# Kernel tuning notes

Measured on AMD Instinct MI355X. Metric: run time of the kernel, lower is better.

Reference implementation:

```python
import jax, jax.numpy as jnp
import numpy as np

POOL_SCALES = (1, 2, 3, 6)
MAX_SCALE = 6


def _seq_ppm(x, w, b):
    """SequencePPM: per-frame PPM with per-frame/per-scale 1x1 conv + ReLU.
    x: [T,B,C,H,W]; w: [T,S,Co,C]; b: [T,S,Co]. Returns [T,B,S*Co,MAX,MAX]."""
    T, B, C, H, W = x.shape
    outs = []
    for si, s in enumerate(POOL_SCALES):
        # AdaptiveAvgPool2d(s): H,W divisible by s -> equal block means
        pooled = x.reshape(T, B, C, s, H // s, s, W // s).mean(axis=(4, 6))  # [T,B,C,s,s]
        conv = jnp.einsum('tbcij,toc->tboij', pooled, w[:, si]) + b[:, si][:, None, :, None, None]
        conv = jax.nn.relu(conv)
        # bilinear upsample to (MAX_SCALE, MAX_SCALE), align_corners=False
        up = jax.image.resize(conv, (T, B, conv.shape[2], MAX_SCALE, MAX_SCALE), method='bilinear')
        outs.append(up)
    return jnp.concatenate(outs, axis=2)  # [T,B,sum(Co),MAX,MAX]


def setup_inputs() -> dict:
    key = jax.random.key(0)
    ks = jax.random.split(key, 8)
    T, B, Ck, Cv, H, W = 4, 2, 256, 512, 96, 96
    S = len(POOL_SCALES)
    return {
        'memory_keys': jax.random.normal(ks[0], (T, B, Ck, H, W), jnp.float32),
        'memory_values': jax.random.normal(ks[1], (T, B, Cv, H, W), jnp.float32),
        'query_key': jax.random.normal(ks[2], (B, Ck, H, W), jnp.float32),
        'query_value': jax.random.normal(ks[3], (B, Cv, H, W), jnp.float32),
        'key_w': jax.random.normal(ks[4], (T, S, Ck // S, Ck), jnp.float32) * (Ck ** -0.5),
        'key_b': jnp.zeros((T, S, Ck // S), jnp.float32),
        'val_w': jax.random.normal(ks[5], (T, S, Cv // S, Cv), jnp.float32) * (Cv ** -0.5),
        'val_b': jnp.zeros((T, S, Cv // S), jnp.float32),
    }


def reference(memory_keys, memory_values, query_key, query_value, key_w, key_b, val_w, val_b):
    T, B, Ck, H, W = memory_keys.shape
    Cv = memory_values.shape[2]
    mk = _seq_ppm(memory_keys, key_w, key_b)      # [T,B,Ck,6,6]
    mv = _seq_ppm(memory_values, val_w, val_b)    # [T,B,Cv,6,6]
    h = w = MAX_SCALE
    M = T * h * w
    # keys: [B, M, Ck] with M ordered (T, h, w)
    mk = jnp.transpose(mk, (1, 0, 3, 4, 2)).reshape(B, M, Ck)
    mv = jnp.transpose(mv, (1, 2, 0, 3, 4)).reshape(B, Cv, M)
    qk = query_key.reshape(B, Ck, H * W)
    att = jnp.einsum('bmc,bcn->bmn', mk, qk) * (Ck ** -0.5)  # matmul_norm=True
    att = jax.nn.softmax(att, axis=1)  # softmax over memory dim M
    mem = jnp.einsum('bvm,bmn->bvn', mv, att).reshape(B, Cv, H, W)
    return jnp.concatenate([query_value, mem], axis=1)  # [B, 2*Cv, H, W]
```

## Files before the change

### kernel.cpp

```cpp
#include <hip/hip_runtime.h>
#include <hip/hip_bf16.h>

#define T_ 4
#define B_ 2
#define CK 256
#define CV 512
#define HH 96
#define WW 96
#define NPIX (HH*WW)
#define M_ 144
#define MP 160

typedef __attribute__((ext_vector_type(8))) short short8;
typedef __attribute__((ext_vector_type(4))) float floatx4;

__device__ __forceinline__ unsigned short f2bf(float f) {
    unsigned int u = __float_as_uint(f);
    u += 0x7FFFu + ((u >> 16) & 1u);
    return (unsigned short)(u >> 16);
}

__global__ __launch_bounds__(256) void pool_kernel(
        const float* __restrict__ keys, const float* __restrict__ vals,
        float* __restrict__ pooledK, float* __restrict__ pooledV) {
    int pid = blockIdx.x;
    const float* src; float* dst;
    if (pid < T_*B_*CK) { src = keys + (size_t)pid * NPIX; dst = pooledK + (size_t)pid * 50; }
    else { int p = pid - T_*B_*CK; src = vals + (size_t)p * NPIX; dst = pooledV + (size_t)p * 50; }

    __shared__ float cm[36];
    int tid = threadIdx.x;
    int wv = tid >> 6, lane = tid & 63;
    int r = lane >> 2, c4 = lane & 3;
    #pragma unroll
    for (int g = 0; g < 9; ++g) {
        int cell = g*4 + wv;
        int cr = cell / 6, cc = cell % 6;
        const float4 v = *reinterpret_cast<const float4*>(src + (cr*16 + r)*WW + cc*16 + c4*4);
        float s = v.x + v.y + v.z + v.w;
        #pragma unroll
        for (int m = 1; m < 64; m <<= 1) s += __shfl_xor(s, m);
        if (lane == 0) cm[cell] = s * (1.0f/256.0f);
    }
    __syncthreads();
    if (tid < 50) {
        float v;
        if (tid == 0) {
            float a = 0.f;
            #pragma unroll
            for (int i = 0; i < 36; ++i) a += cm[i];
            v = a * (1.0f/36.0f);
        } else if (tid < 5) {
            int k = tid - 1; int i = k >> 1, j = k & 1;
            float a = 0.f;
            for (int di = 0; di < 3; ++di)
                for (int dj = 0; dj < 3; ++dj) a += cm[(i*3+di)*6 + (j*3+dj)];
            v = a * (1.0f/9.0f);
        } else if (tid < 14) {
            int k = tid - 5; int i = k / 3, j = k % 3;
            float a = 0.f;
            for (int di = 0; di < 2; ++di)
                for (int dj = 0; dj < 2; ++dj) a += cm[(i*2+di)*6 + (j*2+dj)];
            v = a * 0.25f;
        } else {
            v = cm[tid - 14];
        }
        dst[tid] = v;
    }
}

__global__ __launch_bounds__(256) void conv_kernel(
        const float* __restrict__ pooledK, const float* __restrict__ pooledV,
        const float* __restrict__ key_w, const float* __restrict__ key_b,
        const float* __restrict__ val_w, const float* __restrict__ val_b,
        float* __restrict__ convK, float* __restrict__ convV) {
    int gid = blockIdx.x * 4 + (threadIdx.x >> 6);
    int lane = threadIdx.x & 63;
    const int EK = T_*B_*50*64;
    float acc = 0.f;
    if (gid < EK) {
        int co = gid & 63;
        int pos = (gid >> 6) % 50;
        int tb = gid / (64*50);
        int b = tb & 1, t = tb >> 1;
        int si = (pos == 0) ? 0 : (pos < 5 ? 1 : (pos < 14 ? 2 : 3));
        const float* wrow = key_w + (size_t)((t*4 + si)*64 + co) * CK;
        const float* prow = pooledK + (size_t)((t*B_ + b)*CK) * 50 + pos;
        #pragma unroll
        for (int k = 0; k < 4; ++k) {
            int c = lane + 64*k;
            acc += wrow[c] * prow[(size_t)c * 50];
        }
        #pragma unroll
        for (int m = 1; m < 64; m <<= 1) acc += __shfl_xor(acc, m);
        if (lane == 0) convK[gid] = fmaxf(acc + key_b[(t*4 + si)*64 + co], 0.f);
    } else {
        int g2 = gid - EK;
        int co = g2 & 127;
        int pos = (g2 >> 7) % 50;
        int tb = g2 / (128*50);
        int b = tb & 1, t = tb >> 1;
        int si = (pos == 0) ? 0 : (pos < 5 ? 1 : (pos < 14 ? 2 : 3));
        const float* wrow = val_w + (size_t)((t*4 + si)*128 + co) * CV;
        const float* prow = pooledV + (size_t)((t*B_ + b)*CV) * 50 + pos;
        #pragma unroll
        for (int k = 0; k < 8; ++k) {
            int c = lane + 64*k;
            acc += wrow[c] * prow[(size_t)c * 50];
        }
        #pragma unroll
        for (int m = 1; m < 64; m <<= 1) acc += __shfl_xor(acc, m);
        if (lane == 0) convV[g2] = fmaxf(acc + val_b[(t*4 + si)*128 + co], 0.f);
    }
}

__device__ const int   UP_P0[4][6] = {{0,0,0,0,0,0},{0,0,0,0,1,1},{0,0,0,1,1,2},{0,1,2,3,4,5}};
__device__ const int   UP_P1[4][6] = {{0,0,0,0,0,0},{0,0,1,1,1,1},{0,1,1,2,2,2},{0,1,2,3,4,5}};
__device__ const float UP_W0[4][6] = {{1,1,1,1,1,1},
                                      {1,1,0.66666669f,0.33333334f,1,1},
                                      {1,0.75f,0.25f,0.75f,0.25f,1},
                                      {1,1,1,1,1,1}};
__device__ const float UP_W1[4][6] = {{0,0,0,0,0,0},
                                      {0,0,0.33333334f,0.66666669f,0,0},
                                      {0,0.25f,0.75f,0.25f,0.75f,0},
                                      {0,0,0,0,0,0}};
__device__ const int   UP_OFF[4] = {0,1,5,14};
__device__ const int   UP_S[4]   = {1,2,3,6};

__global__ __launch_bounds__(256) void pack_kernel(
        const float* __restrict__ convK, const float* __restrict__ convV,
        unsigned short* __restrict__ mk_b, unsigned short* __restrict__ mv_b) {
    int F = blockIdx.x * 256 + threadIdx.x;
    const int NMK = B_ * M_ * CK;
    if (F < NMK) {
        int c = F & 255;
        int m = (F >> 8) % M_;
        int b = F / (M_ * 256);
        int t = m / 36, rem = m % 36, y = rem / 6, x = rem % 6;
        int si = c >> 6, co = c & 63;
        int s = UP_S[si], off = UP_OFF[si];
        const float* base = convK + (size_t)((t*B_ + b)*50) * 64 + co;
        int py0 = UP_P0[si][y], py1 = UP_P1[si][y];
        int px0 = UP_P0[si][x], px1 = UP_P1[si][x];
        float wy0 = UP_W0[si][y], wy1 = UP_W1[si][y];
        float wx0 = UP_W0[si][x], wx1 = UP_W1[si][x];
        float v = wy0 * (wx0 * base[(off + py0*s + px0)*64] + wx1 * base[(off + py0*s + px1)*64])
                + wy1 * (wx0 * base[(off + py1*s + px0)*64] + wx1 * base[(off + py1*s + px1)*64]);
        mk_b[F] = f2bf(v);
    } else {
        int G = F - NMK;
        int mp = G % MP;
        int cv = (G / MP) % CV;
        int b = G / (MP * CV);
        if (mp >= M_) { mv_b[G] = 0; return; }
        int m = mp;
        int t = m / 36, rem = m % 36, y = rem / 6, x = rem % 6;
        int si = cv >> 7, co = cv & 127;
        int s = UP_S[si], off = UP_OFF[si];
        const float* base = convV + (size_t)((t*B_ + b)*50) * 128 + co;
        int py0 = UP_P0[si][y], py1 = UP_P1[si][y];
        int px0 = UP_P0[si][x], px1 = UP_P1[si][x];
        float wy0 = UP_W0[si][y], wy1 = UP_W1[si][y];
        float wx0 = UP_W0[si][x], wx1 = UP_W1[si][x];
        float v = wy0 * (wx0 * base[(off + py0*s + px0)*128] + wx1 * base[(off + py0*s + px1)*128])
                + wy1 * (wx0 * base[(off + py1*s + px0)*128] + wx1 * base[(off + py1*s + px1)*128]);
        mv_b[G] = f2bf(v);
    }
}

__global__ __launch_bounds__(256) void attn_kernel(
        const float* __restrict__ qk, const float* __restrict__ qv,
        const unsigned short* __restrict__ mk_b, const unsigned short* __restrict__ mv_b,
        float* __restrict__ out) {
    __shared__ __align__(16) unsigned short qk_s[64 * 264];
    __shared__ __align__(16) unsigned short p_s[64 * 168];

    int blk = blockIdx.x;
    int b = blk / 144;
    int n0 = (blk % 144) * 64;
    int tid = threadIdx.x;

    {
        int nn = tid & 63, cq = tid >> 6;
        const float* qb = qk + (size_t)b * CK * NPIX + n0 + nn;
        for (int k = 0; k < 32; ++k) {
            int c0 = 2 * (cq + 4*k);
            float v0 = qb[(size_t)c0 * NPIX];
            float v1 = qb[(size_t)(c0 + 1) * NPIX];
            unsigned int pk = (unsigned int)f2bf(v0) | ((unsigned int)f2bf(v1) << 16);
            *reinterpret_cast<unsigned int*>(&qk_s[nn*264 + c0]) = pk;
        }
    }
    __syncthreads();

    int w = tid >> 6, l = tid & 63;
    int nl = l & 15, q = l >> 4;

    short8 bq[8];
    #pragma unroll
    for (int kt = 0; kt < 8; ++kt)
        bq[kt] = *reinterpret_cast<const short8*>(&qk_s[(w*16 + nl)*264 + kt*32 + q*8]);

    floatx4 sc[9];
    const unsigned short* mkb = mk_b + (size_t)b * M_ * CK + (size_t)nl * CK + q*8;
    #pragma unroll
    for (int mt = 0; mt < 9; ++mt) {
        floatx4 acc = {0.f, 0.f, 0.f, 0.f};
        const unsigned short* ar = mkb + (size_t)mt * 16 * CK;
        #pragma unroll
        for (int kt = 0; kt < 8; ++kt) {
            short8 a = *reinterpret_cast<const short8*>(ar + kt*32);
            acc = __builtin_amdgcn_mfma_f32_16x16x32_bf16(a, bq[kt], acc, 0, 0, 0);
        }
        sc[mt] = acc;
    }

    float mx = -3.0e38f;
    #pragma unroll
    for (int mt = 0; mt < 9; ++mt)
        #pragma unroll
        for (int r = 0; r < 4; ++r) {
            float tv = sc[mt][r] * 0.0625f;
            sc[mt][r] = tv;
            mx = fmaxf(mx, tv);
        }
    mx = fmaxf(mx, __shfl_xor(mx, 16));
    mx = fmaxf(mx, __shfl_xor(mx, 32));
    float sum = 0.f;
    #pragma unroll
    for (int mt = 0; mt < 9; ++mt)
        #pragma unroll
        for (int r = 0; r < 4; ++r) {
            float e = __expf(sc[mt][r] - mx);
            sc[mt][r] = e;
            sum += e;
        }
    sum += __shfl_xor(sum, 16);
    sum += __shfl_xor(sum, 32);
    float inv = 1.0f / sum;

    unsigned short* pw = &p_s[(w*16 + nl)*168];
    #pragma unroll
    for (int mt = 0; mt < 9; ++mt)
        #pragma unroll
        for (int r = 0; r < 4; ++r)
            pw[mt*16 + q*4 + r] = f2bf(sc[mt][r] * inv);
    #pragma unroll
    for (int r = 0; r < 4; ++r) pw[M_ + q*4 + r] = 0;
    __syncthreads();

    short8 bp[4][5];
    #pragma unroll
    for (int ns = 0; ns < 4; ++ns)
        #pragma unroll
        for (int kt = 0; kt < 5; ++kt)
            bp[ns][kt] = *reinterpret_cast<const short8*>(&p_s[(ns*16 + nl)*168 + kt*32 + q*8]);

    const unsigned short* mvb = mv_b + (size_t)b * CV * MP + (size_t)(w*128 + nl) * MP + q*8;
    float* ob = out + (size_t)(b*1024 + 512 + w*128 + q*4) * NPIX + n0 + nl;
    #pragma unroll
    for (int mt2 = 0; mt2 < 8; ++mt2) {
        short8 af[5];
        const unsigned short* ar = mvb + (size_t)mt2 * 16 * MP;
        #pragma unroll
        for (int kt = 0; kt < 5; ++kt)
            af[kt] = *reinterpret_cast<const short8*>(ar + kt*32);
        #pragma unroll
        for (int ns = 0; ns < 4; ++ns) {
            floatx4 acc = {0.f, 0.f, 0.f, 0.f};
            #pragma unroll
            for (int kt = 0; kt < 5; ++kt)
                acc = __builtin_amdgcn_mfma_f32_16x16x32_bf16(af[kt], bp[ns][kt], acc, 0, 0, 0);
            float* op = ob + (size_t)(mt2*16) * NPIX + ns*16;
            op[0]        = acc[0];
            op[NPIX]     = acc[1];
            op[2*NPIX]   = acc[2];
            op[3*NPIX]   = acc[3];
        }
    }

    {
        int f4 = tid & 15, rr = tid >> 4;
        const float* qvb = qv + (size_t)b * CV * NPIX + n0 + f4*4;
        float* ob2 = out + (size_t)b * 1024 * NPIX + n0 + f4*4;
        for (int it = 0; it < 32; ++it) {
            int cvr = it*16 + rr;
            float4 v = *reinterpret_cast<const float4*>(qvb + (size_t)cvr * NPIX);
            *reinterpret_cast<float4*>(ob2 + (size_t)cvr * NPIX) = v;
        }
    }
}

extern "C" void kernel_launch(void* const* d_in, const int* in_sizes, int n_in,
                              void* d_out, int out_size, void* d_ws, size_t ws_size,
                              hipStream_t stream) {
    const float* keys  = (const float*)d_in[0];
    const float* vals  = (const float*)d_in[1];
    const float* qk    = (const float*)d_in[2];
    const float* qv    = (const float*)d_in[3];
    const float* key_w = (const float*)d_in[4];
    const float* key_b = (const float*)d_in[5];
    const float* val_w = (const float*)d_in[6];
    const float* val_b = (const float*)d_in[7];
    float* out = (float*)d_out;

    char* ws = (char*)d_ws;
    float* pooledK = (float*)(ws + 0);
    float* pooledV = (float*)(ws + 409600);
    float* convK   = (float*)(ws + 1228800);
    float* convV   = (float*)(ws + 1331200);
    unsigned short* mk_b = (unsigned short*)(ws + 1536000);
    unsigned short* mv_b = (unsigned short*)(ws + 1683456);

    hipLaunchKernelGGL(pool_kernel, dim3(T_*B_*(CK+CV)), dim3(256), 0, stream,
                       keys, vals, pooledK, pooledV);
    hipLaunchKernelGGL(conv_kernel, dim3((T_*B_*50*64 + T_*B_*50*128) / 4 / 64), dim3(256), 0, stream,
                       pooledK, pooledV, key_w, key_b, val_w, val_b, convK, convV);
    hipLaunchKernelGGL(pack_kernel, dim3((B_*M_*CK + B_*CV*MP) / 256), dim3(256), 0, stream,
                       convK, convV, mk_b, mv_b);
    hipLaunchKernelGGL(attn_kernel, dim3(B_ * (NPIX/64)), dim3(256), 0, stream,
                       qk, qv, mk_b, mv_b, out);
}
```

Measured before the change: 368.4 us.

## Restructure pooling reads, transpose pooled layout, vectorize qk load, split qv copy

```diff
diff --git a/kernel.cpp b/kernel.cpp
--- a/kernel.cpp
+++ b/kernel.cpp
@@ -20,52 +20,78 @@
     return (unsigned short)(u >> 16);
 }
 
-__global__ __launch_bounds__(256) void pool_kernel(
+__global__ __launch_bounds__(384) void pool_kernel(
         const float* __restrict__ keys, const float* __restrict__ vals,
         float* __restrict__ pooledK, float* __restrict__ pooledV) {
     int pid = blockIdx.x;
-    const float* src; float* dst;
-    if (pid < T_*B_*CK) { src = keys + (size_t)pid * NPIX; dst = pooledK + (size_t)pid * 50; }
-    else { int p = pid - T_*B_*CK; src = vals + (size_t)p * NPIX; dst = pooledV + (size_t)p * 50; }
-
+    const float* src; float* dstbase; int Cstride;
+    if (pid < T_*B_*CK) {
+        int tb = pid / CK, c = pid % CK;
+        src = keys + (size_t)pid * NPIX;
+        dstbase = pooledK + (size_t)tb * 50 * CK + c;
+        Cstride = CK;
+    } else {
+        int p = pid - T_*B_*CK;
+        int tb = p / CV, c = p % CV;
+        src = vals + (size_t)p * NPIX;
+        dstbase = pooledV + (size_t)tb * 50 * CV + c;
+        Cstride = CV;
+    }
+
+    int t = threadIdx.x;
+    int g = t % 24, rb = t / 24;
+    const float* p0 = src + rb*WW + g*4;
+
+    float4 v[6];
+    #pragma unroll
+    for (int k = 0; k < 6; ++k)
+        v[k] = *reinterpret_cast<const float4*>(p0 + (size_t)k*16*WW);
+
+    __shared__ float lds[6*16*24];
+    #pragma unroll
+    for (int k = 0; k < 6; ++k)
+        lds[(k*16 + rb)*24 + g] = v[k].x + v[k].y + v[k].z + v[k].w;
+    __syncthreads();
+
+    __shared__ float part[144];
+    if (t < 144) {
+        int cidx = t >> 2, p = t & 3;
+        int k = cidx / 6, cc = cidx % 6;
+        float a = 0.f;
+        #pragma unroll
+        for (int r2 = 0; r2 < 16; ++r2)
+            a += lds[(k*16 + r2)*24 + cc*4 + p];
+        part[t] = a;
+    }
+    __syncthreads();
     __shared__ float cm[36];
-    int tid = threadIdx.x;
-    int wv = tid >> 6, lane = tid & 63;
-    int r = lane >> 2, c4 = lane & 3;
-    #pragma unroll
-    for (int g = 0; g < 9; ++g) {
-        int cell = g*4 + wv;
-        int cr = cell / 6, cc = cell % 6;
-        const float4 v = *reinterpret_cast<const float4*>(src + (cr*16 + r)*WW + cc*16 + c4*4);
-        float s = v.x + v.y + v.z + v.w;
-        #pragma unroll
-        for (int m = 1; m < 64; m <<= 1) s += __shfl_xor(s, m);
-        if (lane == 0) cm[cell] = s * (1.0f/256.0f);
-    }
-    __syncthreads();
-    if (tid < 50) {
-        float v;
-        if (tid == 0) {
+    if (t < 36)
+        cm[t] = (part[t*4] + part[t*4+1] + part[t*4+2] + part[t*4+3]) * (1.0f/256.0f);
+    __syncthreads();
+
+    if (t < 50) {
+        float val;
+        if (t == 0) {
             float a = 0.f;
             #pragma unroll
             for (int i = 0; i < 36; ++i) a += cm[i];
-            v = a * (1.0f/36.0f);
-        } else if (tid < 5) {
-            int k = tid - 1; int i = k >> 1, j = k & 1;
+            val = a * (1.0f/36.0f);
+        } else if (t < 5) {
+            int k = t - 1; int i = k >> 1, j = k & 1;
             float a = 0.f;
             for (int di = 0; di < 3; ++di)
                 for (int dj = 0; dj < 3; ++dj) a += cm[(i*3+di)*6 + (j*3+dj)];
-            v = a * (1.0f/9.0f);
-        } else if (tid < 14) {
-            int k = tid - 5; int i = k / 3, j = k % 3;
+            val = a * (1.0f/9.0f);
+        } else if (t < 14) {
+            int k = t - 5; int i = k / 3, j = k % 3;
             float a = 0.f;
             for (int di = 0; di < 2; ++di)
                 for (int dj = 0; dj < 2; ++dj) a += cm[(i*2+di)*6 + (j*2+dj)];
-            v = a * 0.25f;
+            val = a * 0.25f;
         } else {
-            v = cm[tid - 14];
-        }
-        dst[tid] = v;
+            val = cm[t - 14];
+        }
+        dstbase[t * Cstride] = val;
     }
 }
 
@@ -85,11 +111,11 @@
         int b = tb & 1, t = tb >> 1;
         int si = (pos == 0) ? 0 : (pos < 5 ? 1 : (pos < 14 ? 2 : 3));
         const float* wrow = key_w + (size_t)((t*4 + si)*64 + co) * CK;
-        const float* prow = pooledK + (size_t)((t*B_ + b)*CK) * 50 + pos;
+        const float* prow = pooledK + (size_t)(tb*50 + pos) * CK;
         #pragma unroll
         for (int k = 0; k < 4; ++k) {
             int c = lane + 64*k;
-            acc += wrow[c] * prow[(size_t)c * 50];
+            acc += wrow[c] * prow[c];
         }
         #pragma unroll
         for (int m = 1; m < 64; m <<= 1) acc += __shfl_xor(acc, m);
@@ -102,11 +128,11 @@
         int b = tb & 1, t = tb >> 1;
         int si = (pos == 0) ? 0 : (pos < 5 ? 1 : (pos < 14 ? 2 : 3));
         const float* wrow = val_w + (size_t)((t*4 + si)*128 + co) * CV;
-        const float* prow = pooledV + (size_t)((t*B_ + b)*CV) * 50 + pos;
+        const float* prow = pooledV + (size_t)(tb*50 + pos) * CV;
         #pragma unroll
         for (int k = 0; k < 8; ++k) {
             int c = lane + 64*k;
-            acc += wrow[c] * prow[(size_t)c * 50];
+            acc += wrow[c] * prow[c];
         }
         #pragma unroll
         for (int m = 1; m < 64; m <<= 1) acc += __shfl_xor(acc, m);
@@ -169,7 +195,7 @@
 }
 
 __global__ __launch_bounds__(256) void attn_kernel(
-        const float* __restrict__ qk, const float* __restrict__ qv,
+        const float* __restrict__ qk,
         const unsigned short* __restrict__ mk_b, const unsigned short* __restrict__ mv_b,
         float* __restrict__ out) {
     __shared__ __align__(16) unsigned short qk_s[64 * 264];
@@ -181,14 +207,17 @@
     int tid = threadIdx.x;
 
     {
-        int nn = tid & 63, cq = tid >> 6;
-        const float* qb = qk + (size_t)b * CK * NPIX + n0 + nn;
-        for (int k = 0; k < 32; ++k) {
-            int c0 = 2 * (cq + 4*k);
-            float v0 = qb[(size_t)c0 * NPIX];
-            float v1 = qb[(size_t)(c0 + 1) * NPIX];
-            unsigned int pk = (unsigned int)f2bf(v0) | ((unsigned int)f2bf(v1) << 16);
-            *reinterpret_cast<unsigned int*>(&qk_s[nn*264 + c0]) = pk;
+        int px = (tid & 15) * 4;
+        int c0 = tid >> 4;
+        const float* qb = qk + (size_t)b * CK * NPIX + n0 + px;
+        #pragma unroll
+        for (int k = 0; k < 16; ++k) {
+            int c = c0 + 16*k;
+            float4 v = *reinterpret_cast<const float4*>(qb + (size_t)c * NPIX);
+            qk_s[(px+0)*264 + c] = f2bf(v.x);
+            qk_s[(px+1)*264 + c] = f2bf(v.y);
+            qk_s[(px+2)*264 + c] = f2bf(v.z);
+            qk_s[(px+3)*264 + c] = f2bf(v.w);
         }
     }
     __syncthreads();
@@ -278,17 +307,15 @@
             op[3*NPIX]   = acc[3];
         }
     }
-
-    {
-        int f4 = tid & 15, rr = tid >> 4;
-        const float* qvb = qv + (size_t)b * CV * NPIX + n0 + f4*4;
-        float* ob2 = out + (size_t)b * 1024 * NPIX + n0 + f4*4;
-        for (int it = 0; it < 32; ++it) {
-            int cvr = it*16 + rr;
-            float4 v = *reinterpret_cast<const float4*>(qvb + (size_t)cvr * NPIX);
-            *reinterpret_cast<float4*>(ob2 + (size_t)cvr * NPIX) = v;
-        }
-    }
+}
+
+__global__ __launch_bounds__(256) void qvcopy_kernel(
+        const float* __restrict__ qv, float* __restrict__ out) {
+    size_t off = ((size_t)blockIdx.x * 256 + threadIdx.x) * 4;
+    size_t b1 = (size_t)CV * NPIX;
+    size_t dst = off + (off >= b1 ? b1 : 0);
+    float4 v = *reinterpret_cast<const float4*>(qv + off);
+    *reinterpret_cast<float4*>(out + dst) = v;
 }
 
 extern "C" void kernel_launch(void* const* d_in, const int* in_sizes, int n_in,
@@ -312,12 +339,14 @@
     unsigned short* mk_b = (unsigned short*)(ws + 1536000);
     unsigned short* mv_b = (unsigned short*)(ws + 1683456);
 
-    hipLaunchKernelGGL(pool_kernel, dim3(T_*B_*(CK+CV)), dim3(256), 0, stream,
+    hipLaunchKernelGGL(pool_kernel, dim3(T_*B_*(CK+CV)), dim3(384), 0, stream,
                        keys, vals, pooledK, pooledV);
     hipLaunchKernelGGL(conv_kernel, dim3((T_*B_*50*64 + T_*B_*50*128) / 4 / 64), dim3(256), 0, stream,
                        pooledK, pooledV, key_w, key_b, val_w, val_b, convK, convV);
     hipLaunchKernelGGL(pack_kernel, dim3((B_*M_*CK + B_*CV*MP) / 256), dim3(256), 0, stream,
                        convK, convV, mk_b, mv_b);
     hipLaunchKernelGGL(attn_kernel, dim3(B_ * (NPIX/64)), dim3(256), 0, stream,
-                       qk, qv, mk_b, mv_b, out);
-}
+                       qk, mk_b, mv_b, out);
+    hipLaunchKernelGGL(qvcopy_kernel, dim3(B_*CV*NPIX/4/256), dim3(256), 0, stream,
+                       qv, out);
+}
```

Result: faster. 359.3 us (-2.5%).
